# Kernel optimization log

Hardware: AMD Instinct MI355X
Metric: run time of the kernel (lower is better)

The kernel has to match this reference:

```python
import jax, jax.numpy as jnp
import numpy as np

N = 50000      # nodes per graph batch (per side)
E = 600000     # edges per side
B = 4096       # number of graphs (drug pairs)
D = 128        # node_dim == hidden_dim
K = 128        # kge_dim
R = 86         # rel_total
L = 3          # n_iter
EPS = 1e-5


def setup_inputs() -> dict:
    key = jax.random.key(0)
    ks = jax.random.split(key, 16)
    inp = {}
    inp["x1"] = jax.random.normal(ks[0], (N, D), jnp.float32)
    inp["x2"] = jax.random.normal(ks[1], (N, D), jnp.float32)
    inp["edge_index1"] = jax.random.randint(ks[2], (2, E), 0, N)
    inp["edge_index2"] = jax.random.randint(ks[3], (2, E), 0, N)
    inp["batch1"] = jnp.sort(jax.random.randint(ks[4], (N,), 0, B))
    inp["batch2"] = jnp.sort(jax.random.randint(ks[5], (N,), 0, B))
    inp["rel"] = jax.random.randint(ks[6], (B,), 0, R)
    # SAGEConv params, stacked over L layers (all [D,D] since node_dim==hidden_dim)
    sc = 0.05
    inp["Wl"] = jax.random.normal(ks[7], (L, D, D), jnp.float32) * sc   # lin on aggregated neighbors (has bias)
    inp["bl"] = jnp.zeros((L, D), jnp.float32)
    inp["Wr"] = jax.random.normal(ks[8], (L, D, D), jnp.float32) * sc   # root (self) lin, no bias
    # BatchNorm (eval mode: running stats)
    inp["bn_gamma"] = jnp.ones((L, D), jnp.float32)
    inp["bn_beta"] = jnp.zeros((L, D), jnp.float32)
    inp["bn_mean"] = jnp.zeros((L, D), jnp.float32)
    inp["bn_var"] = jnp.ones((L, D), jnp.float32)
    # relation embedding + final MLP
    inp["kge"] = jax.random.normal(ks[9], (R, K), jnp.float32)
    inp["W1"] = jax.random.normal(ks[10], (2 * D + K, D), jnp.float32) * sc
    inp["b1"] = jnp.zeros((D,), jnp.float32)
    inp["W2"] = jax.random.normal(ks[11], (D, 1), jnp.float32) * sc
    inp["b2"] = jnp.zeros((1,), jnp.float32)
    return inp


def _gnn(x, edge_index, Wl, bl, Wr, g, b, m, v):
    src, dst = edge_index[0], edge_index[1]
    deg = jax.ops.segment_sum(jnp.ones((E,), x.dtype), dst, num_segments=N)
    deg = jnp.maximum(deg, 1.0)[:, None]
    for i in range(L):
        agg = jax.ops.segment_sum(x[src], dst, num_segments=N) / deg  # mean aggregation
        h = agg @ Wl[i] + bl[i] + x @ Wr[i]                           # SAGEConv
        h = (h - m[i]) * (g[i] / jnp.sqrt(v[i] + EPS)) + b[i]         # BN (eval)
        x = jax.nn.relu(h)                                            # dropout = identity (eval)
    return x


def reference(x1, edge_index1, batch1, x2, edge_index2, batch2, rel,
              Wl, bl, Wr, bn_gamma, bn_beta, bn_mean, bn_var,
              kge, W1, b1, W2, b2):
    h1 = _gnn(x1, edge_index1, Wl, bl, Wr, bn_gamma, bn_beta, bn_mean, bn_var)
    h2 = _gnn(x2, edge_index2, Wl, bl, Wr, bn_gamma, bn_beta, bn_mean, bn_var)
    p1 = jax.ops.segment_sum(h1, batch1, num_segments=B)  # global_add_pool
    p2 = jax.ops.segment_sum(h2, batch2, num_segments=B)
    r = kge[rel]                                          # [B, K]
    z = jnp.concatenate([p1, p2, r], axis=-1)             # [B, 2D+K]
    h = jax.nn.relu(z @ W1 + b1)
    out = h @ W2 + b2
    return out.reshape(-1)
```

## Files before the change

### kernel.cpp

```cpp
#include <hip/hip_runtime.h>

#define NN 50000
#define NE 600000
#define NB 4096
#define DD 128
#define EPSV 1e-5f
#define NBKT 196
#define NCHUNK 256
#define CHSZ ((NE + NCHUNK - 1) / NCHUNK)

typedef __bf16 bf16x8 __attribute__((ext_vector_type(8)));
typedef float f32x4 __attribute__((ext_vector_type(4)));
typedef float f32x2 __attribute__((ext_vector_type(2)));

__device__ inline unsigned short f2bf(float f) {
    unsigned u = __float_as_uint(f);
    u = (u + 0x7FFFu + ((u >> 16) & 1u)) >> 16;
    return (unsigned short)u;
}
__device__ inline float bf2f(unsigned short h) {
    return __uint_as_float(((unsigned)h) << 16);
}

__global__ void k_cvt(const float* __restrict__ x1, const float* __restrict__ x2,
                      unsigned short* __restrict__ xh, unsigned short* __restrict__ xl) {
    int i = blockIdx.x * 256 + threadIdx.x;
    if (i >= 2 * NN * 32) return;
    const float* x = (i < NN * 32) ? x1 : x2;
    int j = (i < NN * 32) ? i : i - NN * 32;
    float4 v = ((const float4*)x)[j];
    ushort4 h, l;
    h.x = f2bf(v.x); l.x = f2bf(v.x - bf2f(h.x));
    h.y = f2bf(v.y); l.y = f2bf(v.y - bf2f(h.y));
    h.z = f2bf(v.z); l.z = f2bf(v.z - bf2f(h.z));
    h.w = f2bf(v.w); l.w = f2bf(v.w - bf2f(h.w));
    ((ushort4*)xh)[i] = h;
    ((ushort4*)xl)[i] = l;
}

__global__ void k_wcvt(const float* __restrict__ Wl, const float* __restrict__ Wr,
                       const float* __restrict__ W1,
                       unsigned short* __restrict__ wfp, unsigned* __restrict__ w1p) {
    int t = blockIdx.x * 256 + threadIdx.x;
    if (t < 3 * 128 * 256) {
        int k = t & 255;
        int n = (t >> 8) & 127;
        int l = t >> 15;
        float w = (k < 128) ? Wl[l * 16384 + k * 128 + n] : Wr[l * 16384 + (k - 128) * 128 + n];
        unsigned short h = f2bf(w);
        unsigned short lo = f2bf(w - bf2f(h));
        int c = k >> 5, kk = k & 31;
        size_t base = (size_t)l * 65536 + (size_t)c * 8192 + n * 32 + kk;
        wfp[base] = h;
        wfp[base + 4096] = lo;
    } else if (t < 3 * 128 * 256 + 128 * 384) {
        int u = t - 3 * 128 * 256;
        int n = u / 384;
        int k = u - n * 384;
        float w = W1[k * 128 + n];
        unsigned short h = f2bf(w);
        unsigned short l = f2bf(w - bf2f(h));
        w1p[u] = ((unsigned)h << 16) | (unsigned)l;
    }
}

__global__ void k_hist(const int* __restrict__ d0, const int* __restrict__ d1,
                       int* __restrict__ bcnt) {
    int side = (blockIdx.x >= NCHUNK) ? 1 : 0;
    int c = blockIdx.x - side * NCHUNK;
    const int* dst = side ? d1 : d0;
    int tid = threadIdx.x;
    __shared__ int h[NBKT];
    for (int i = tid; i < NBKT; i += 256) h[i] = 0;
    __syncthreads();
    int e0 = c * CHSZ, e1 = min(e0 + CHSZ, NE);
    for (int e = e0 + tid; e < e1; e += 256) atomicAdd(&h[dst[e] >> 8], 1);
    __syncthreads();
    int* bc = bcnt + ((size_t)side * NCHUNK + c) * NBKT;
    for (int i = tid; i < NBKT; i += 256) bc[i] = h[i];
}

__global__ void k_s1(int* __restrict__ bcnt, int* __restrict__ btot) {
    int side = (blockIdx.x >= NBKT) ? 1 : 0;
    int b = blockIdx.x - side * NBKT;
    int tid = threadIdx.x;
    int idx = ((size_t)side * NCHUNK + tid) * NBKT + b;
    int v = bcnt[idx];
    int lane = tid & 63, wv = tid >> 6;
    int x = v;
#pragma unroll
    for (int off = 1; off < 64; off <<= 1) {
        int y = __shfl_up(x, off, 64);
        if (lane >= off) x += y;
    }
    __shared__ int ws4[4];
    if (lane == 63) ws4[wv] = x;
    __syncthreads();
    int add = 0;
#pragma unroll
    for (int w = 0; w < 4; w++)
        if (w < wv) add += ws4[w];
    int incl = x + add;
    bcnt[idx] = incl - v;
    if (tid == 255) btot[side * NBKT + b] = incl;
}

__global__ void k_s2(const int* __restrict__ btot, int* __restrict__ bbase,
                     int* __restrict__ ptrC) {
    int side = blockIdx.x;
    int tid = threadIdx.x;
    int v = (tid < NBKT) ? btot[side * NBKT + tid] : 0;
    int lane = tid & 63, wv = tid >> 6;
    int x = v;
#pragma unroll
    for (int off = 1; off < 64; off <<= 1) {
        int y = __shfl_up(x, off, 64);
        if (lane >= off) x += y;
    }
    __shared__ int ws4[4];
    if (lane == 63) ws4[wv] = x;
    __syncthreads();
    int add = 0;
#pragma unroll
    for (int w = 0; w < 4; w++)
        if (w < wv) add += ws4[w];
    int incl = x + add;
    if (tid < NBKT) bbase[side * NBKT + tid] = incl - v;
    if (tid == 0 && side == 1) ptrC[2 * NN] = 2 * NE;
}

__global__ void k_part(const int* __restrict__ s0, const int* __restrict__ d0,
                       const int* __restrict__ s1, const int* __restrict__ d1,
                       const int* __restrict__ bcnt, const int* __restrict__ bbase,
                       int* __restrict__ part) {
    int side = (blockIdx.x >= NCHUNK) ? 1 : 0;
    int c = blockIdx.x - side * NCHUNK;
    const int* src = side ? s1 : s0;
    const int* dst = side ? d1 : d0;
    int tid = threadIdx.x;
    __shared__ int off[NBKT];
    const int* bc = bcnt + ((size_t)side * NCHUNK + c) * NBKT;
    for (int i = tid; i < NBKT; i += 256) off[i] = bbase[side * NBKT + i] + bc[i];
    __syncthreads();
    int e0 = c * CHSZ, e1 = min(e0 + CHSZ, NE);
    int* P = part + (size_t)side * NE;
    int soff = side * NN;
    for (int e = e0 + tid; e < e1; e += 256) {
        int d = dst[e];
        int pos = atomicAdd(&off[d >> 8], 1);
        P[pos] = ((src[e] + soff) << 8) | (d & 255);
    }
}

__global__ void k_csr(const int* __restrict__ part, const int* __restrict__ bbase,
                      int* __restrict__ ptrC, float* __restrict__ invdC,
                      int* __restrict__ csrC) {
    int side = (blockIdx.x >= NBKT) ? 1 : 0;
    int b = blockIdx.x - side * NBKT;
    int tid = threadIdx.x;
    const int* P = part + (size_t)side * NE;
    int base = bbase[side * NBKT + b];
    int endp = (b == NBKT - 1) ? NE : bbase[side * NBKT + b + 1];
    __shared__ int cnt[256];
    cnt[tid] = 0;
    __syncthreads();
    for (int e = base + tid; e < endp; e += 256) atomicAdd(&cnt[P[e] & 255], 1);
    __syncthreads();
    int v = cnt[tid];
    int lane = tid & 63, wv = tid >> 6;
    int x = v;
#pragma unroll
    for (int off = 1; off < 64; off <<= 1) {
        int y = __shfl_up(x, off, 64);
        if (lane >= off) x += y;
    }
    __shared__ int ws4[4];
    if (lane == 63) ws4[wv] = x;
    __syncthreads();
    int add = 0;
#pragma unroll
    for (int w = 0; w < 4; w++)
        if (w < wv) add += ws4[w];
    int excl = x + add - v;
    int node = (b << 8) + tid;
    if (node < NN) {
        ptrC[side * NN + node] = side * NE + base + excl;
        invdC[side * NN + node] = 1.0f / (float)(v > 1 ? v : 1);
    }
    __syncthreads();
    cnt[tid] = excl;
    __syncthreads();
    for (int e = base + tid; e < endp; e += 256) {
        int p = P[e];
        int pos = atomicAdd(&cnt[p & 255], 1);
        csrC[(size_t)side * NE + base + pos] = p >> 8;
    }
}

__global__ void k_gather(const unsigned short* __restrict__ xh, const int* __restrict__ ptr,
                         const int* __restrict__ csr, const float* __restrict__ invd,
                         unsigned short* __restrict__ aggH) {
    int wid = threadIdx.x >> 6;
    int lane = threadIdx.x & 63;
    int q = lane >> 4;
    int c = lane & 15;
    int n = blockIdx.x * 4 + wid;
    if (n >= 2 * NN) return;
    int beg = ptr[n], end = ptr[n + 1];
    float id = invd[n];
    f32x2 a2[4];
#pragma unroll
    for (int k = 0; k < 4; k++) a2[k] = (f32x2){0.f, 0.f};

    for (int base = beg; base < end; base += 64) {
        int cnt = min(end - base, 64);
        int idxv = csr[base + min(lane, cnt - 1)];
        for (int e0 = 0; e0 < cnt; e0 += 8) {
            int eA = e0 + q;
            int eB = e0 + 4 + q;
            int iA = __shfl(idxv, eA, 64);
            int iB = __shfl(idxv, eB, 64);
            f32x2 wA2 = (eA < cnt) ? (f32x2){1.f, 1.f} : (f32x2){0.f, 0.f};
            f32x2 wB2 = (eB < cnt) ? (f32x2){1.f, 1.f} : (f32x2){0.f, 0.f};
            uint4 vA = *(const uint4*)(xh + (((unsigned)iA << 7) + (c << 3)));
            uint4 vB = *(const uint4*)(xh + (((unsigned)iB << 7) + (c << 3)));
            a2[0] += wA2 * (f32x2){__uint_as_float(vA.x << 16), __uint_as_float(vA.x & 0xffff0000u)};
            a2[1] += wA2 * (f32x2){__uint_as_float(vA.y << 16), __uint_as_float(vA.y & 0xffff0000u)};
            a2[2] += wA2 * (f32x2){__uint_as_float(vA.z << 16), __uint_as_float(vA.z & 0xffff0000u)};
            a2[3] += wA2 * (f32x2){__uint_as_float(vA.w << 16), __uint_as_float(vA.w & 0xffff0000u)};
            a2[0] += wB2 * (f32x2){__uint_as_float(vB.x << 16), __uint_as_float(vB.x & 0xffff0000u)};
            a2[1] += wB2 * (f32x2){__uint_as_float(vB.y << 16), __uint_as_float(vB.y & 0xffff0000u)};
            a2[2] += wB2 * (f32x2){__uint_as_float(vB.z << 16), __uint_as_float(vB.z & 0xffff0000u)};
            a2[3] += wB2 * (f32x2){__uint_as_float(vB.w << 16), __uint_as_float(vB.w & 0xffff0000u)};
        }
    }
    float a[8];
    a[0] = a2[0][0]; a[1] = a2[0][1];
    a[2] = a2[1][0]; a[3] = a2[1][1];
    a[4] = a2[2][0]; a[5] = a2[2][1];
    a[6] = a2[3][0]; a[7] = a2[3][1];
#pragma unroll
    for (int k = 0; k < 8; k++) {
        a[k] += __shfl_xor(a[k], 16, 64);
        a[k] += __shfl_xor(a[k], 32, 64);
    }
    if (q == 0) {
        unsigned short h0 = f2bf(a[0] * id), h1 = f2bf(a[1] * id);
        unsigned short h2 = f2bf(a[2] * id), h3 = f2bf(a[3] * id);
        unsigned short h4 = f2bf(a[4] * id), h5 = f2bf(a[5] * id);
        unsigned short h6 = f2bf(a[6] * id), h7 = f2bf(a[7] * id);
        uint4 o;
        o.x = (unsigned)h0 | ((unsigned)h1 << 16);
        o.y = (unsigned)h2 | ((unsigned)h3 << 16);
        o.z = (unsigned)h4 | ((unsigned)h5 << 16);
        o.w = (unsigned)h6 | ((unsigned)h7 << 16);
        *(uint4*)(aggH + (size_t)n * DD + c * 8) = o;
    }
}

__launch_bounds__(256)
__global__ void k_gemmL(const unsigned short* __restrict__ AH,
                        const unsigned short* __restrict__ XH, const unsigned short* __restrict__ XL,
                        const unsigned short* __restrict__ wfp,
                        const float* __restrict__ bl, const float* __restrict__ g,
                        const float* __restrict__ be, const float* __restrict__ mn,
                        const float* __restrict__ vr,
                        unsigned short* __restrict__ OH, unsigned short* __restrict__ OL,
                        float* __restrict__ Of, int f32out) {
    __shared__ __align__(16) unsigned short sA[2][128 * 40];
    __shared__ __align__(16) unsigned short sW[2][128 * 40];
    int tid = threadIdx.x;
    int lane = tid & 63, w = tid >> 6;
    int fm = lane & 15, kq = lane >> 4;
    int m0 = blockIdx.x * 128;
    int wr = (w & 1) * 64;
    int wn = (w >> 1) * 64;

    int srow[2], sseg[2];
    size_t gbase[2];
    bool sok[2];
#pragma unroll
    for (int i = 0; i < 2; i++) {
        int s = tid + 256 * i;
        srow[i] = s >> 2;
        sseg[i] = s & 3;
        int grow = m0 + srow[i];
        sok[i] = grow < 2 * NN;
        gbase[i] = (size_t)grow * DD + sseg[i] * 8;
    }

    uint4 ph[2], pl[2];
#pragma unroll
    for (int i = 0; i < 2; i++)
        ph[i] = sok[i] ? *(const uint4*)(AH + gbase[i]) : make_uint4(0, 0, 0, 0);

    float scv[4], shv[4];
#pragma unroll
    for (int nt = 0; nt < 4; nt++) {
        int jj = wn + nt * 16 + fm;
        float s = g[jj] * rsqrtf(vr[jj] + EPSV);
        scv[nt] = s;
        shv[nt] = (bl[jj] - mn[jj]) * s + be[jj];
    }

    f32x4 acc[4][4];
#pragma unroll
    for (int i = 0; i < 4; i++)
#pragma unroll
        for (int j = 0; j < 4; j++) acc[i][j] = (f32x4){0.f, 0.f, 0.f, 0.f};

#pragma unroll
    for (int c = 0; c < 8; c++) {
        int isA = (c < 4);
        if (c > 0) __syncthreads();
#pragma unroll
        for (int i = 0; i < 2; i++) {
            *(uint4*)&sA[0][srow[i] * 40 + sseg[i] * 8] = ph[i];
            if (!isA) *(uint4*)&sA[1][srow[i] * 40 + sseg[i] * 8] = pl[i];
        }
        const unsigned short* wb = wfp + (size_t)c * 8192;
#pragma unroll
        for (int i = 0; i < 2; i++) {
            int s = tid + 256 * i;
            *(uint4*)&sW[0][srow[i] * 40 + sseg[i] * 8] = *(const uint4*)(wb + s * 8);
            *(uint4*)&sW[1][srow[i] * 40 + sseg[i] * 8] = *(const uint4*)(wb + 4096 + s * 8);
        }
        if (c < 7) {
            int cn = c + 1;
            const unsigned short* SH = (cn < 4) ? AH : XH;
            size_t koff = (size_t)(cn & 3) * 32;
#pragma unroll
            for (int i = 0; i < 2; i++) {
                ph[i] = sok[i] ? *(const uint4*)(SH + gbase[i] + koff) : make_uint4(0, 0, 0, 0);
                if (cn >= 4)
                    pl[i] = sok[i] ? *(const uint4*)(XL + gbase[i] + koff) : make_uint4(0, 0, 0, 0);
            }
        }
        __syncthreads();

        bf16x8 ah[4], al[4];
#pragma unroll
        for (int mt = 0; mt < 4; mt++) {
            int r = wr + mt * 16 + fm;
            ah[mt] = *(const bf16x8*)&sA[0][r * 40 + kq * 8];
            if (!isA) al[mt] = *(const bf16x8*)&sA[1][r * 40 + kq * 8];
        }
#pragma unroll
        for (int nt = 0; nt < 4; nt++) {
            int nr = wn + nt * 16 + fm;
            bf16x8 wh = *(const bf16x8*)&sW[0][nr * 40 + kq * 8];
            bf16x8 wl = *(const bf16x8*)&sW[1][nr * 40 + kq * 8];
#pragma unroll
            for (int mt = 0; mt < 4; mt++) {
                acc[mt][nt] = __builtin_amdgcn_mfma_f32_16x16x32_bf16(ah[mt], wh, acc[mt][nt], 0, 0, 0);
                acc[mt][nt] = __builtin_amdgcn_mfma_f32_16x16x32_bf16(ah[mt], wl, acc[mt][nt], 0, 0, 0);
                if (!isA)
                    acc[mt][nt] = __builtin_amdgcn_mfma_f32_16x16x32_bf16(al[mt], wh, acc[mt][nt], 0, 0, 0);
            }
        }
    }

#pragma unroll
    for (int mt = 0; mt < 4; mt++) {
#pragma unroll
        for (int r = 0; r < 4; r++) {
            int grow = m0 + wr + mt * 16 + kq * 4 + r;
            if (grow < 2 * NN) {
#pragma unroll
                for (int nt = 0; nt < 4; nt++) {
                    int gcol = wn + nt * 16 + fm;
                    float o = fmaxf(acc[mt][nt][r] * scv[nt] + shv[nt], 0.f);
                    if (f32out) {
                        Of[(size_t)grow * DD + gcol] = o;
                    } else {
                        unsigned short h = f2bf(o);
                        OH[(size_t)grow * DD + gcol] = h;
                        OL[(size_t)grow * DD + gcol] = f2bf(o - bf2f(h));
                    }
                }
            }
        }
    }
}

__launch_bounds__(128)
__global__ void k_pool2z(const float* __restrict__ cf, const int* __restrict__ bt1,
                         const int* __restrict__ bt2, const int* __restrict__ rel,
                         const float* __restrict__ kge,
                         unsigned short* __restrict__ zh, unsigned short* __restrict__ zl) {
    int side = (blockIdx.x >= NB) ? 1 : 0;
    int b = blockIdx.x - side * NB;
    const int* batch = side ? bt2 : bt1;
    const float* h = cf + (size_t)side * NN * DD;
    __shared__ int sr[2];
    if (threadIdx.x < 2) {
        int target = b + (int)threadIdx.x;
        int lo = 0, hi = NN;
        while (lo < hi) {
            int mid = (lo + hi) >> 1;
            if (batch[mid] < target) lo = mid + 1; else hi = mid;
        }
        sr[threadIdx.x] = lo;
    }
    __syncthreads();
    int beg = sr[0], end = sr[1];
    int t = threadIdx.x;
    float acc = 0.f;
    for (int r = beg; r < end; r++) acc += h[(size_t)r * DD + t];
    size_t zo = (size_t)b * 384 + side * 128 + t;
    unsigned short hh = f2bf(acc);
    zh[zo] = hh;
    zl[zo] = f2bf(acc - bf2f(hh));
    if (side == 0) {
        float kv = kge[(size_t)rel[b] * 128 + t];
        size_t zk = (size_t)b * 384 + 256 + t;
        unsigned short kh = f2bf(kv);
        zh[zk] = kh;
        zl[zk] = f2bf(kv - bf2f(kh));
    }
}

__launch_bounds__(256)
__global__ void k_mlp2(const unsigned short* __restrict__ zh, const unsigned short* __restrict__ zl,
                       const unsigned* __restrict__ w1p,
                       const float* __restrict__ b1, const float* __restrict__ W2,
                       const float* __restrict__ b2, float* __restrict__ out) {
    __shared__ __align__(16) unsigned short sZ[2][32 * 40];
    __shared__ __align__(16) unsigned short sW[2][128 * 40];
    __shared__ float hpart[32][4];
    int tid = threadIdx.x;
    int m0 = blockIdx.x * 32;
    int lane = tid & 63, w = tid >> 6;
    int fm = lane & 15, q = lane >> 4;
    int wn = w * 32;

    f32x4 acc[2][2];
#pragma unroll
    for (int i = 0; i < 2; i++)
#pragma unroll
        for (int j = 0; j < 2; j++) acc[i][j] = (f32x4){0.f, 0.f, 0.f, 0.f};

    for (int c = 0; c < 12; c++) {
        int k0 = c * 32;
        __syncthreads();
        {
            int row = tid >> 3, seg = tid & 7;
            size_t off = (size_t)(m0 + row) * 384 + k0 + seg * 4;
            *(ushort4*)&sZ[0][row * 40 + seg * 4] = *(const ushort4*)(zh + off);
            *(ushort4*)&sZ[1][row * 40 + seg * 4] = *(const ushort4*)(zl + off);
        }
#pragma unroll
        for (int i = 0; i < 4; i++) {
            int u = tid + 256 * i;
            int row = u >> 3, seg = u & 7;
            uint4 val = *(const uint4*)(w1p + (size_t)row * 384 + k0 + seg * 4);
            ushort4 hi, lo;
            hi.x = val.x >> 16; hi.y = val.y >> 16; hi.z = val.z >> 16; hi.w = val.w >> 16;
            lo.x = val.x & 0xFFFF; lo.y = val.y & 0xFFFF; lo.z = val.z & 0xFFFF; lo.w = val.w & 0xFFFF;
            *(ushort4*)&sW[0][row * 40 + seg * 4] = hi;
            *(ushort4*)&sW[1][row * 40 + seg * 4] = lo;
        }
        __syncthreads();
        bf16x8 zfh[2], zfl[2];
#pragma unroll
        for (int mt = 0; mt < 2; mt++) {
            int r = mt * 16 + fm;
            zfh[mt] = *(const bf16x8*)&sZ[0][r * 40 + q * 8];
            zfl[mt] = *(const bf16x8*)&sZ[1][r * 40 + q * 8];
        }
#pragma unroll
        for (int nt = 0; nt < 2; nt++) {
            int nr = wn + nt * 16 + fm;
            bf16x8 wh = *(const bf16x8*)&sW[0][nr * 40 + q * 8];
            bf16x8 wl = *(const bf16x8*)&sW[1][nr * 40 + q * 8];
#pragma unroll
            for (int mt = 0; mt < 2; mt++) {
                acc[mt][nt] = __builtin_amdgcn_mfma_f32_16x16x32_bf16(zfh[mt], wh, acc[mt][nt], 0, 0, 0);
                acc[mt][nt] = __builtin_amdgcn_mfma_f32_16x16x32_bf16(zfh[mt], wl, acc[mt][nt], 0, 0, 0);
                acc[mt][nt] = __builtin_amdgcn_mfma_f32_16x16x32_bf16(zfl[mt], wh, acc[mt][nt], 0, 0, 0);
            }
        }
    }

    float b1v[2], w2v[2];
#pragma unroll
    for (int nt = 0; nt < 2; nt++) {
        int col = wn + nt * 16 + fm;
        b1v[nt] = b1[col];
        w2v[nt] = W2[col];
    }
#pragma unroll
    for (int mt = 0; mt < 2; mt++) {
#pragma unroll
        for (int r = 0; r < 4; r++) {
            float val = 0.f;
#pragma unroll
            for (int nt = 0; nt < 2; nt++)
                val += fmaxf(acc[mt][nt][r] + b1v[nt], 0.f) * w2v[nt];
#pragma unroll
            for (int m = 1; m < 16; m <<= 1) val += __shfl_xor(val, m, 64);
            if (fm == 0) hpart[mt * 16 + q * 4 + r][w] = val;
        }
    }
    __syncthreads();
    if (tid < 32)
        out[m0 + tid] = hpart[tid][0] + hpart[tid][1] + hpart[tid][2] + hpart[tid][3] + b2[0];
}

extern "C" void kernel_launch(void* const* d_in, const int* in_sizes, int n_in,
                              void* d_out, int out_size, void* d_ws, size_t ws_size,
                              hipStream_t stream) {
    const float* x1  = (const float*)d_in[0];
    const float* x2  = (const float*)d_in[1];
    const int*   ei1 = (const int*)d_in[2];
    const int*   ei2 = (const int*)d_in[3];
    const int*   bt1 = (const int*)d_in[4];
    const int*   bt2 = (const int*)d_in[5];
    const int*   rel = (const int*)d_in[6];
    const float* Wl  = (const float*)d_in[7];
    const float* bl  = (const float*)d_in[8];
    const float* Wr  = (const float*)d_in[9];
    const float* g   = (const float*)d_in[10];
    const float* be  = (const float*)d_in[11];
    const float* mn  = (const float*)d_in[12];
    const float* vr  = (const float*)d_in[13];
    const float* kge = (const float*)d_in[14];
    const float* W1  = (const float*)d_in[15];
    const float* b1v = (const float*)d_in[16];
    const float* W2  = (const float*)d_in[17];
    const float* b2v = (const float*)d_in[18];

    char* ws = (char*)d_ws;
    size_t off = 0;
    auto alloc = [&](size_t bytes) {
        void* p = ws + off;
        off += (bytes + 255) & ~(size_t)255;
        return p;
    };
    const size_t PL = (size_t)2 * NN * DD;
    unsigned short* xbufH = (unsigned short*)alloc(PL * 2);
    unsigned short* xbufL = (unsigned short*)alloc(PL * 2);
    unsigned short* obufH = (unsigned short*)alloc(PL * 2);
    unsigned short* obufL = (unsigned short*)alloc(PL * 2);
    unsigned short* aggH  = (unsigned short*)alloc(PL * 2);
    unsigned short* wfp   = (unsigned short*)alloc((size_t)3 * 65536 * 2);
    unsigned* w1p  = (unsigned*)alloc((size_t)128 * 384 * 4);
    unsigned short* zh = (unsigned short*)alloc((size_t)NB * 384 * 2);
    unsigned short* zl = (unsigned short*)alloc((size_t)NB * 384 * 2);
    int*   bcnt    = (int*)alloc((size_t)2 * NCHUNK * NBKT * 4);
    int*   btot    = (int*)alloc((size_t)2 * NBKT * 4);
    int*   bbase   = (int*)alloc((size_t)2 * NBKT * 4);
    int*   part    = (int*)alloc((size_t)2 * NE * 4);
    int*   ptrC    = (int*)alloc((size_t)(2 * NN + 1) * 4);
    float* invdC   = (float*)alloc((size_t)2 * NN * 4);
    int*   csrC    = (int*)alloc((size_t)2 * NE * 4);
    if (off > ws_size) return;

    float* cf = (float*)obufH;

    const int nbCvt   = 12500;
    const int nbNode4 = (2 * NN + 3) / 4;
    const int nbGemmL = (2 * NN + 127) / 128;
    const int nbW     = (3 * 128 * 256 + 128 * 384 + 255) / 256;

    k_wcvt<<<nbW, 256, 0, stream>>>(Wl, Wr, W1, wfp, w1p);

    k_hist<<<2 * NCHUNK, 256, 0, stream>>>(ei1 + NE, ei2 + NE, bcnt);
    k_s1<<<2 * NBKT, 256, 0, stream>>>(bcnt, btot);
    k_s2<<<2, 256, 0, stream>>>(btot, bbase, ptrC);
    k_part<<<2 * NCHUNK, 256, 0, stream>>>(ei1, ei1 + NE, ei2, ei2 + NE, bcnt, bbase, part);
    k_csr<<<2 * NBKT, 256, 0, stream>>>(part, bbase, ptrC, invdC, csrC);

    k_cvt<<<nbCvt, 256, 0, stream>>>(x1, x2, xbufH, xbufL);

    k_gather<<<nbNode4, 256, 0, stream>>>(xbufH, ptrC, csrC, invdC, aggH);
    k_gemmL<<<nbGemmL, 256, 0, stream>>>(aggH, xbufH, xbufL, wfp, bl, g, be, mn, vr,
                                         obufH, obufL, (float*)nullptr, 0);
    k_gather<<<nbNode4, 256, 0, stream>>>(obufH, ptrC, csrC, invdC, aggH);
    k_gemmL<<<nbGemmL, 256, 0, stream>>>(aggH, obufH, obufL, wfp + 65536, bl + 128, g + 128,
                                         be + 128, mn + 128, vr + 128,
                                         xbufH, xbufL, (float*)nullptr, 0);
    k_gather<<<nbNode4, 256, 0, stream>>>(xbufH, ptrC, csrC, invdC, aggH);
    k_gemmL<<<nbGemmL, 256, 0, stream>>>(aggH, xbufH, xbufL, wfp + 131072, bl + 256, g + 256,
                                         be + 256, mn + 256, vr + 256,
                                         (unsigned short*)nullptr, (unsigned short*)nullptr, cf, 1);

    k_pool2z<<<2 * NB, 128, 0, stream>>>(cf, bt1, bt2, rel, kge, zh, zl);
    k_mlp2<<<NB / 32, 256, 0, stream>>>(zh, zl, w1p, b1v, W2, b2v, (float*)d_out);
}
```

Baseline: 447.9 us.

## Merge prep kernels, swizzle GEMM LDS layout, prefetch weight tiles into registers

Folds the x conversion, weight conversion and edge histogram into a single launch, which removes two kernel launches and lets the three independent jobs run at the same time. In the layer GEMM, the padded LDS rows of stride 40 become unpadded stride-32 rows with an XOR swizzle, cutting LDS use while aiming to keep bank-conflict-free access. Weight tiles for the next K-chunk are now loaded into registers ahead of time, as the activations already were, so global weight loads overlap compute. The cost is higher register pressure, and a single combined kernel with branches of uneven weight.

```diff
diff --git a/kernel.cpp b/kernel.cpp
--- a/kernel.cpp
+++ b/kernel.cpp
@@ -22,62 +22,63 @@
     return __uint_as_float(((unsigned)h) << 16);
 }
 
-__global__ void k_cvt(const float* __restrict__ x1, const float* __restrict__ x2,
-                      unsigned short* __restrict__ xh, unsigned short* __restrict__ xl) {
-    int i = blockIdx.x * 256 + threadIdx.x;
-    if (i >= 2 * NN * 32) return;
-    const float* x = (i < NN * 32) ? x1 : x2;
-    int j = (i < NN * 32) ? i : i - NN * 32;
-    float4 v = ((const float4*)x)[j];
-    ushort4 h, l;
-    h.x = f2bf(v.x); l.x = f2bf(v.x - bf2f(h.x));
-    h.y = f2bf(v.y); l.y = f2bf(v.y - bf2f(h.y));
-    h.z = f2bf(v.z); l.z = f2bf(v.z - bf2f(h.z));
-    h.w = f2bf(v.w); l.w = f2bf(v.w - bf2f(h.w));
-    ((ushort4*)xh)[i] = h;
-    ((ushort4*)xl)[i] = l;
-}
-
-__global__ void k_wcvt(const float* __restrict__ Wl, const float* __restrict__ Wr,
+__global__ void k_prep(const float* __restrict__ x1, const float* __restrict__ x2,
+                       unsigned short* __restrict__ xh, unsigned short* __restrict__ xl,
+                       const float* __restrict__ Wl, const float* __restrict__ Wr,
                        const float* __restrict__ W1,
-                       unsigned short* __restrict__ wfp, unsigned* __restrict__ w1p) {
-    int t = blockIdx.x * 256 + threadIdx.x;
-    if (t < 3 * 128 * 256) {
-        int k = t & 255;
-        int n = (t >> 8) & 127;
-        int l = t >> 15;
-        float w = (k < 128) ? Wl[l * 16384 + k * 128 + n] : Wr[l * 16384 + (k - 128) * 128 + n];
-        unsigned short h = f2bf(w);
-        unsigned short lo = f2bf(w - bf2f(h));
-        int c = k >> 5, kk = k & 31;
-        size_t base = (size_t)l * 65536 + (size_t)c * 8192 + n * 32 + kk;
-        wfp[base] = h;
-        wfp[base + 4096] = lo;
-    } else if (t < 3 * 128 * 256 + 128 * 384) {
-        int u = t - 3 * 128 * 256;
-        int n = u / 384;
-        int k = u - n * 384;
-        float w = W1[k * 128 + n];
-        unsigned short h = f2bf(w);
-        unsigned short l = f2bf(w - bf2f(h));
-        w1p[u] = ((unsigned)h << 16) | (unsigned)l;
-    }
-}
-
-__global__ void k_hist(const int* __restrict__ d0, const int* __restrict__ d1,
+                       unsigned short* __restrict__ wfp, unsigned* __restrict__ w1p,
+                       const int* __restrict__ d0, const int* __restrict__ d1,
                        int* __restrict__ bcnt) {
-    int side = (blockIdx.x >= NCHUNK) ? 1 : 0;
-    int c = blockIdx.x - side * NCHUNK;
-    const int* dst = side ? d1 : d0;
-    int tid = threadIdx.x;
     __shared__ int h[NBKT];
-    for (int i = tid; i < NBKT; i += 256) h[i] = 0;
-    __syncthreads();
-    int e0 = c * CHSZ, e1 = min(e0 + CHSZ, NE);
-    for (int e = e0 + tid; e < e1; e += 256) atomicAdd(&h[dst[e] >> 8], 1);
-    __syncthreads();
-    int* bc = bcnt + ((size_t)side * NCHUNK + c) * NBKT;
-    for (int i = tid; i < NBKT; i += 256) bc[i] = h[i];
+    int b = blockIdx.x;
+    int tid = threadIdx.x;
+    if (b < 12500) {
+        int i = b * 256 + tid;
+        const float* x = (i < NN * 32) ? x1 : x2;
+        int j = (i < NN * 32) ? i : i - NN * 32;
+        float4 v = ((const float4*)x)[j];
+        ushort4 hh, ll;
+        hh.x = f2bf(v.x); ll.x = f2bf(v.x - bf2f(hh.x));
+        hh.y = f2bf(v.y); ll.y = f2bf(v.y - bf2f(hh.y));
+        hh.z = f2bf(v.z); ll.z = f2bf(v.z - bf2f(hh.z));
+        hh.w = f2bf(v.w); ll.w = f2bf(v.w - bf2f(hh.w));
+        ((ushort4*)xh)[i] = hh;
+        ((ushort4*)xl)[i] = ll;
+    } else if (b < 12500 + 576) {
+        int t = (b - 12500) * 256 + tid;
+        if (t < 3 * 128 * 256) {
+            int k = t & 255;
+            int n = (t >> 8) & 127;
+            int l = t >> 15;
+            float w = (k < 128) ? Wl[l * 16384 + k * 128 + n] : Wr[l * 16384 + (k - 128) * 128 + n];
+            unsigned short hh = f2bf(w);
+            unsigned short lo = f2bf(w - bf2f(hh));
+            int c = k >> 5, kk = k & 31;
+            size_t base = (size_t)l * 65536 + (size_t)c * 8192 + n * 32 + kk;
+            wfp[base] = hh;
+            wfp[base + 4096] = lo;
+        } else if (t < 3 * 128 * 256 + 128 * 384) {
+            int u = t - 3 * 128 * 256;
+            int n = u / 384;
+            int k = u - n * 384;
+            float w = W1[k * 128 + n];
+            unsigned short hh = f2bf(w);
+            unsigned short ll = f2bf(w - bf2f(hh));
+            w1p[u] = ((unsigned)hh << 16) | (unsigned)ll;
+        }
+    } else {
+        int hb = b - 13076;
+        int side = (hb >= NCHUNK) ? 1 : 0;
+        int c = hb - side * NCHUNK;
+        const int* dst = side ? d1 : d0;
+        for (int i = tid; i < NBKT; i += 256) h[i] = 0;
+        __syncthreads();
+        int e0 = c * CHSZ, e1 = min(e0 + CHSZ, NE);
+        for (int e = e0 + tid; e < e1; e += 256) atomicAdd(&h[dst[e] >> 8], 1);
+        __syncthreads();
+        int* bc = bcnt + ((size_t)side * NCHUNK + c) * NBKT;
+        for (int i = tid; i < NBKT; i += 256) bc[i] = h[i];
+    }
 }
 
 __global__ void k_s1(int* __restrict__ bcnt, int* __restrict__ btot) {
@@ -267,32 +268,37 @@
                         const float* __restrict__ vr,
                         unsigned short* __restrict__ OH, unsigned short* __restrict__ OL,
                         float* __restrict__ Of, int f32out) {
-    __shared__ __align__(16) unsigned short sA[2][128 * 40];
-    __shared__ __align__(16) unsigned short sW[2][128 * 40];
+    __shared__ __align__(16) unsigned short sA[2][128 * 32];
+    __shared__ __align__(16) unsigned short sW[2][128 * 32];
     int tid = threadIdx.x;
     int lane = tid & 63, w = tid >> 6;
     int fm = lane & 15, kq = lane >> 4;
     int m0 = blockIdx.x * 128;
     int wr = (w & 1) * 64;
     int wn = (w >> 1) * 64;
-
-    int srow[2], sseg[2];
+    int ksw = kq ^ ((fm >> 1) & 3);
+
+    int ldsoff[2], sfull[2];
     size_t gbase[2];
     bool sok[2];
 #pragma unroll
     for (int i = 0; i < 2; i++) {
         int s = tid + 256 * i;
-        srow[i] = s >> 2;
-        sseg[i] = s & 3;
-        int grow = m0 + srow[i];
+        int row = s >> 2, seg = s & 3;
+        sfull[i] = s;
+        ldsoff[i] = row * 32 + (seg ^ ((row >> 1) & 3)) * 8;
+        int grow = m0 + row;
         sok[i] = grow < 2 * NN;
-        gbase[i] = (size_t)grow * DD + sseg[i] * 8;
-    }
-
-    uint4 ph[2], pl[2];
-#pragma unroll
-    for (int i = 0; i < 2; i++)
+        gbase[i] = (size_t)grow * DD + seg * 8;
+    }
+
+    uint4 ph[2], plr[2], pwh[2], pwl[2];
+#pragma unroll
+    for (int i = 0; i < 2; i++) {
         ph[i] = sok[i] ? *(const uint4*)(AH + gbase[i]) : make_uint4(0, 0, 0, 0);
+        pwh[i] = *(const uint4*)(wfp + sfull[i] * 8);
+        pwl[i] = *(const uint4*)(wfp + 4096 + sfull[i] * 8);
+    }
 
     float scv[4], shv[4];
 #pragma unroll
@@ -315,25 +321,23 @@
         if (c > 0) __syncthreads();
 #pragma unroll
         for (int i = 0; i < 2; i++) {
-            *(uint4*)&sA[0][srow[i] * 40 + sseg[i] * 8] = ph[i];
-            if (!isA) *(uint4*)&sA[1][srow[i] * 40 + sseg[i] * 8] = pl[i];
-        }
-        const unsigned short* wb = wfp + (size_t)c * 8192;
-#pragma unroll
-        for (int i = 0; i < 2; i++) {
-            int s = tid + 256 * i;
-            *(uint4*)&sW[0][srow[i] * 40 + sseg[i] * 8] = *(const uint4*)(wb + s * 8);
-            *(uint4*)&sW[1][srow[i] * 40 + sseg[i] * 8] = *(const uint4*)(wb + 4096 + s * 8);
+            *(uint4*)&sA[0][ldsoff[i]] = ph[i];
+            if (!isA) *(uint4*)&sA[1][ldsoff[i]] = plr[i];
+            *(uint4*)&sW[0][ldsoff[i]] = pwh[i];
+            *(uint4*)&sW[1][ldsoff[i]] = pwl[i];
         }
         if (c < 7) {
             int cn = c + 1;
             const unsigned short* SH = (cn < 4) ? AH : XH;
             size_t koff = (size_t)(cn & 3) * 32;
+            const unsigned short* wbn = wfp + (size_t)cn * 8192;
 #pragma unroll
             for (int i = 0; i < 2; i++) {
                 ph[i] = sok[i] ? *(const uint4*)(SH + gbase[i] + koff) : make_uint4(0, 0, 0, 0);
                 if (cn >= 4)
-                    pl[i] = sok[i] ? *(const uint4*)(XL + gbase[i] + koff) : make_uint4(0, 0, 0, 0);
+                    plr[i] = sok[i] ? *(const uint4*)(XL + gbase[i] + koff) : make_uint4(0, 0, 0, 0);
+                pwh[i] = *(const uint4*)(wbn + sfull[i] * 8);
+                pwl[i] = *(const uint4*)(wbn + 4096 + sfull[i] * 8);
             }
         }
         __syncthreads();
@@ -342,14 +346,14 @@
 #pragma unroll
         for (int mt = 0; mt < 4; mt++) {
             int r = wr + mt * 16 + fm;
-            ah[mt] = *(const bf16x8*)&sA[0][r * 40 + kq * 8];
-            if (!isA) al[mt] = *(const bf16x8*)&sA[1][r * 40 + kq * 8];
+            ah[mt] = *(const bf16x8*)&sA[0][r * 32 + ksw * 8];
+            if (!isA) al[mt] = *(const bf16x8*)&sA[1][r * 32 + ksw * 8];
         }
 #pragma unroll
         for (int nt = 0; nt < 4; nt++) {
             int nr = wn + nt * 16 + fm;
-            bf16x8 wh = *(const bf16x8*)&sW[0][nr * 40 + kq * 8];
-            bf16x8 wl = *(const bf16x8*)&sW[1][nr * 40 + kq * 8];
+            bf16x8 wh = *(const bf16x8*)&sW[0][nr * 32 + ksw * 8];
+            bf16x8 wl = *(const bf16x8*)&sW[1][nr * 32 + ksw * 8];
 #pragma unroll
             for (int mt = 0; mt < 4; mt++) {
                 acc[mt][nt] = __builtin_amdgcn_mfma_f32_16x16x32_bf16(ah[mt], wh, acc[mt][nt], 0, 0, 0);
@@ -558,20 +562,17 @@
 
     float* cf = (float*)obufH;
 
-    const int nbCvt   = 12500;
+    const int nbPrep  = 12500 + 576 + 512;
     const int nbNode4 = (2 * NN + 3) / 4;
     const int nbGemmL = (2 * NN + 127) / 128;
-    const int nbW     = (3 * 128 * 256 + 128 * 384 + 255) / 256;
-
-    k_wcvt<<<nbW, 256, 0, stream>>>(Wl, Wr, W1, wfp, w1p);
-
-    k_hist<<<2 * NCHUNK, 256, 0, stream>>>(ei1 + NE, ei2 + NE, bcnt);
+
+    k_prep<<<nbPrep, 256, 0, stream>>>(x1, x2, xbufH, xbufL, Wl, Wr, W1, wfp, w1p,
+                                       ei1 + NE, ei2 + NE, bcnt);
+
     k_s1<<<2 * NBKT, 256, 0, stream>>>(bcnt, btot);
     k_s2<<<2, 256, 0, stream>>>(btot, bbase, ptrC);
     k_part<<<2 * NCHUNK, 256, 0, stream>>>(ei1, ei1 + NE, ei2, ei2 + NE, bcnt, bbase, part);
     k_csr<<<2 * NBKT, 256, 0, stream>>>(part, bbase, ptrC, invdC, csrC);
-
-    k_cvt<<<nbCvt, 256, 0, stream>>>(x1, x2, xbufH, xbufL);
 
     k_gather<<<nbNode4, 256, 0, stream>>>(xbufH, ptrC, csrC, invdC, aggH);
     k_gemmL<<<nbGemmL, 256, 0, stream>>>(aggH, xbufH, xbufL, wfp, bl, g, be, mn, vr,
```

Measured after the change: 493.7 us. +10.2%, slower.
